# Performance work log

Hardware: AMD Instinct MI355X
Metric: run time of the kernel (lower is better)

## Reference

```python
import jax, jax.numpy as jnp
import numpy as np

B, N, D, H, DEPTH = 2, 2048, 768, 12, 4
DH = D // H
SCALE = DH ** -0.5
EPS = 1e-5
FF = 4 * D


def layer_norm(x, w, b):
    m = jnp.mean(x, axis=-1, keepdims=True)
    v = jnp.mean((x - m) ** 2, axis=-1, keepdims=True)
    return (x - m) * jax.lax.rsqrt(v + EPS) * w + b


def to_heads(t):  # [b, n, D] -> [b, H, n, DH]
    b, n, _ = t.shape
    return t.reshape(b, n, H, DH).transpose(0, 2, 1, 3)


def merge_heads(t):  # [b, H, n, DH] -> [b, n, D]
    b, h, n, dh = t.shape
    return t.transpose(0, 2, 1, 3).reshape(b, n, D)


def attend(q, k, v, bias):
    s = jnp.einsum('bhid,bhjd->bhij', q, k) * SCALE + bias
    a = jax.nn.softmax(s, axis=-1)
    return merge_heads(jnp.einsum('bhij,bhjd->bhid', a, v))


def setup_inputs():
    key = jax.random.key(0)
    ks = iter(jax.random.split(key, 16))

    def p(shape, scale=0.02):
        return jax.random.normal(next(ks), shape, dtype=jnp.float32) * scale

    inp = {
        'x': jax.random.normal(next(ks), (B, N, D), dtype=jnp.float32),
        'context': jax.random.normal(next(ks), (B, N, D), dtype=jnp.float32),
        'relative_position_bias': jax.random.normal(next(ks), (1, H, N, N), dtype=jnp.float32) * 0.02,
        # self-attn params (stacked over depth)
        'ln1_w': jnp.ones((DEPTH, D), jnp.float32), 'ln1_b': jnp.zeros((DEPTH, D), jnp.float32),
        'w_qkv': p((DEPTH, D, 3 * D)),
        'w_so': p((DEPTH, D, D)), 'b_so': jnp.zeros((DEPTH, D), jnp.float32),
        # cross-attn params (shared LN applied to x and context, as in source)
        'ln2_w': jnp.ones((DEPTH, D), jnp.float32), 'ln2_b': jnp.zeros((DEPTH, D), jnp.float32),
        'w_q': p((DEPTH, D, D)), 'w_k': p((DEPTH, D, D)), 'w_v': p((DEPTH, D, D)),
        'w_co': p((DEPTH, D, D)), 'b_co': jnp.zeros((DEPTH, D), jnp.float32),
        # FFN params
        'ln3_w': jnp.ones((DEPTH, D), jnp.float32), 'ln3_b': jnp.zeros((DEPTH, D), jnp.float32),
        'w_f1': p((DEPTH, D, FF)), 'b_f1': jnp.zeros((DEPTH, FF), jnp.float32),
        'w_f2': p((DEPTH, FF, D)), 'b_f2': jnp.zeros((DEPTH, D), jnp.float32),
        # final norm
        'lnout_w': jnp.ones((D,), jnp.float32), 'lnout_b': jnp.zeros((D,), jnp.float32),
    }
    return inp


def reference(x, context, relative_position_bias,
              ln1_w, ln1_b, w_qkv, w_so, b_so,
              ln2_w, ln2_b, w_q, w_k, w_v, w_co, b_co,
              ln3_w, ln3_b, w_f1, b_f1, w_f2, b_f2,
              lnout_w, lnout_b):
    bias = relative_position_bias
    for i in range(DEPTH):
        # self-attention block (pre-norm, residual)
        xn = layer_norm(x, ln1_w[i], ln1_b[i])
        q, k, v = jnp.split(xn @ w_qkv[i], 3, axis=-1)
        o = attend(to_heads(q), to_heads(k), to_heads(v), bias)
        x = o @ w_so[i] + b_so[i] + x
        # cross-attention block (input_norm shared for x and context)
        xn = layer_norm(x, ln2_w[i], ln2_b[i])
        cn = layer_norm(context, ln2_w[i], ln2_b[i])
        o = attend(to_heads(xn @ w_q[i]), to_heads(cn @ w_k[i]), to_heads(cn @ w_v[i]), bias)
        x = o @ w_co[i] + b_co[i] + x
        # FFN block
        xn = layer_norm(x, ln3_w[i], ln3_b[i])
        h = jax.nn.gelu(xn @ w_f1[i] + b_f1[i], approximate=False)
        x = h @ w_f2[i] + b_f2[i] + x
    return layer_norm(x, lnout_w, lnout_b)
```

## Files before the change

### kernel.cpp

```cpp
#include <hip/hip_runtime.h>
#include <cstdint>
#include <cstddef>

#define DEV static __device__ __forceinline__

typedef float  f32x4 __attribute__((ext_vector_type(4)));
typedef short  s16x8 __attribute__((ext_vector_type(8)));
typedef unsigned short u16;
typedef unsigned short u16x2 __attribute__((ext_vector_type(2)));
typedef unsigned short u16x4 __attribute__((ext_vector_type(4)));
typedef unsigned short u16x8 __attribute__((ext_vector_type(8)));
typedef __bf16 bf16x8 __attribute__((ext_vector_type(8)));

#define LOG2E 1.4426950408889634f
#define QSCALE_CONST 0.18033688011112042f

DEV float bf2f(u16 v){ union { unsigned u; float f; } x; x.u = ((unsigned)v) << 16; return x.f; }
DEV u16 f2bf(float f){ return __builtin_bit_cast(u16, (__bf16)f); }

DEV float fexp2(float x){
#if __has_builtin(__builtin_amdgcn_exp2f)
  return __builtin_amdgcn_exp2f(x);
#else
  return exp2f(x);
#endif
}

DEV f32x4 mfma16(s16x8 a, s16x8 b, f32x4 c){
  return __builtin_amdgcn_mfma_f32_16x16x32_bf16(
      __builtin_bit_cast(bf16x8, a), __builtin_bit_cast(bf16x8, b), c, 0, 0, 0);
}

DEV void gld16(const void* g, void* l){
  __builtin_amdgcn_global_load_lds(
      (const __attribute__((address_space(1))) void*)(uintptr_t)g,
      (__attribute__((address_space(3))) void*)(unsigned)(uintptr_t)l,
      16, 0, 0);
}

__global__ void __launch_bounds__(256)
transpose_cvt(const float* __restrict__ src, u16* __restrict__ dst, int K, int N,
              size_t dzstride){
  int z = blockIdx.z;
  src += (size_t)z * K * N;
  dst += (size_t)z * dzstride;
  __shared__ float t[32][33];
  int n0 = blockIdx.x * 32, k0 = blockIdx.y * 32;
#pragma unroll
  for (int i = 0; i < 4; ++i)
    t[threadIdx.y + 8*i][threadIdx.x] = src[(size_t)(k0 + threadIdx.y + 8*i) * N + n0 + threadIdx.x];
  __syncthreads();
#pragma unroll
  for (int i = 0; i < 4; ++i)
    dst[(size_t)(n0 + threadIdx.y + 8*i) * K + k0 + threadIdx.x] = f2bf(t[threadIdx.x][threadIdx.y + 8*i]);
}

__global__ void __launch_bounds__(256)
cvt_biasT(const float* __restrict__ in, u16* __restrict__ out){
  const int kvt = blockIdx.x, qt = blockIdx.y, h = blockIdx.z, tid = threadIdx.x;
  const int q  = qt * 64 + ((tid >> 6) << 4) + (tid & 15);
  const int c0 = kvt * 64 + ((tid >> 4) & 3) * 4;
  const float* src = in + ((size_t)h * 2048 + q) * 2048;
  u16x8 o0, o1;
#pragma unroll
  for (int mi = 0; mi < 4; ++mi){
    f32x4 v = *(const f32x4*)(src + c0 + mi * 16);
#pragma unroll
    for (int r = 0; r < 4; ++r){
      u16 bv = f2bf(v[r] * LOG2E);
      if (mi < 2) o0[(mi & 1) * 4 + r] = bv; else o1[(mi & 1) * 4 + r] = bv;
    }
  }
  u16* dst = out + ((size_t)(h * 32 + qt) * 32 + kvt) * 4096 + tid * 16;
  *(u16x8*)dst = o0;
  *(u16x8*)(dst + 8) = o1;
}

__global__ void __launch_bounds__(256)
lnv(const float* __restrict__ x, const float* __restrict__ w, const float* __restrict__ b,
    u16* __restrict__ out){
  const int wv = threadIdx.x >> 6, lane = threadIdx.x & 63;
  const float* wz = w + blockIdx.y * 768;
  const float* bz = b + blockIdx.y * 768;
  out += (size_t)blockIdx.y * 4096 * 768;
  const int row = blockIdx.x * 4 + wv;
  const float* xr = x + (size_t)row * 768;
  f32x4 t[3]; float s = 0.f, s2 = 0.f;
#pragma unroll
  for (int c = 0; c < 3; ++c){
    t[c] = *(const f32x4*)(xr + c * 256 + lane * 4);
#pragma unroll
    for (int j = 0; j < 4; ++j){ s += t[c][j]; s2 += t[c][j] * t[c][j]; }
  }
#pragma unroll
  for (int off = 1; off < 64; off <<= 1){ s += __shfl_xor(s, off); s2 += __shfl_xor(s2, off); }
  float m = s * (1.f/768.f);
  float rstd = rsqrtf(s2 * (1.f/768.f) - m * m + 1e-5f);
#pragma unroll
  for (int c = 0; c < 3; ++c){
    const int col = c * 256 + lane * 4;
    f32x4 wv4 = *(const f32x4*)(wz + col);
    f32x4 bv4 = *(const f32x4*)(bz + col);
    u16x4 o;
#pragma unroll
    for (int j = 0; j < 4; ++j) o[j] = f2bf((t[c][j] - m) * rstd * wv4[j] + bv4[j]);
    *(u16x4*)(out + (size_t)row * 768 + col) = o;
  }
}

template<typename OUT>
__global__ void __launch_bounds__(256)
red_ln(const float* __restrict__ p, const float* __restrict__ biasrow,
       float* __restrict__ xbuf, OUT* __restrict__ out,
       const float* __restrict__ lw, const float* __restrict__ lb){
  const int wv = threadIdx.x >> 6, lane = threadIdx.x & 63;
  const int row = blockIdx.x * 4 + wv;
  const float* p0 = p + (size_t)row * 768;
  const float* p1 = p0 + 4096ll * 768;
  float* xr = xbuf + (size_t)row * 768;
  f32x4 t[3]; float s = 0.f, s2 = 0.f;
#pragma unroll
  for (int c = 0; c < 3; ++c){
    const int col = c * 256 + lane * 4;
    f32x4 v0 = *(const f32x4*)(p0 + col);
    f32x4 v1 = *(const f32x4*)(p1 + col);
    f32x4 bv = *(const f32x4*)(biasrow + col);
    f32x4 xv = *(const f32x4*)(xr + col);
    f32x4 v = v0 + v1 + bv + xv;
    *(f32x4*)(xr + col) = v;
    t[c] = v;
#pragma unroll
    for (int j = 0; j < 4; ++j){ s += v[j]; s2 += v[j] * v[j]; }
  }
#pragma unroll
  for (int off = 1; off < 64; off <<= 1){ s += __shfl_xor(s, off); s2 += __shfl_xor(s2, off); }
  float m = s * (1.f/768.f);
  float rstd = rsqrtf(s2 * (1.f/768.f) - m * m + 1e-5f);
#pragma unroll
  for (int c = 0; c < 3; ++c){
    const int col = c * 256 + lane * 4;
    f32x4 wv4 = *(const f32x4*)(lw + col);
    f32x4 bv4 = *(const f32x4*)(lb + col);
    if constexpr (sizeof(OUT) == 2){
      u16x4 o;
#pragma unroll
      for (int j = 0; j < 4; ++j) o[j] = f2bf((t[c][j] - m) * rstd * wv4[j] + bv4[j]);
      *(u16x4*)((u16*)out + (size_t)row * 768 + col) = o;
    } else {
      f32x4 o;
#pragma unroll
      for (int j = 0; j < 4; ++j) o[j] = (t[c][j] - m) * rstd * wv4[j] + bv4[j];
      *(f32x4*)((float*)out + (size_t)row * 768 + col) = o;
    }
  }
}

template<int BM, int BN, int EPI>
__global__ void __launch_bounds__(256)
gemm_bf16(const u16* __restrict__ A, int lda, const u16* __restrict__ Bt, int ldb,
          int nk, u16* __restrict__ Cb, float* __restrict__ Cf, int ldc,
          const float* __restrict__ bias,
          const u16* __restrict__ A2, const u16* __restrict__ Bt2){
  constexpr int MT = BM / 32, NT = BN / 32;
  __shared__ u16 As[2][BM * 32];
  __shared__ u16 Bs[2][BN * 32];
  float colscale = 1.0f;
  if constexpr (EPI == 4){
    const int z = blockIdx.z;
    if (z == 0){ colscale = QSCALE_CONST; }
    else { A = A2; Bt = Bt2 + (size_t)(z - 1) * 768 * 768; }
    Cb += z * 768;
  }
  if constexpr (EPI == 5){
    const int z = blockIdx.z;
    A  += (size_t)z * nk * 32;
    Bt += (size_t)z * nk * 32;
    Cf += (size_t)z * 4096 * 768;
  }
  const int tid = threadIdx.x, w = tid >> 6, lane = tid & 63;
  const int l16 = lane & 15, g = lane >> 4;
  const int m0 = blockIdx.x * BM, n0 = blockIdx.y * BN;
  const int wm = (w >> 1) * (BM / 2), wn = (w & 1) * (BN / 2);
  f32x4 acc[MT][NT] = {};

  const u16* a0 = A + (size_t)(m0 + (tid >> 2)) * lda + (tid & 3) * 8;
  const u16* a1 = (BM == 128) ? A + (size_t)(m0 + (tid >> 2) + 64) * lda + (tid & 3) * 8 : nullptr;
  const u16* b0 = Bt + (size_t)(n0 + (tid >> 2)) * ldb + (tid & 3) * 8;
  const u16* b1 = (BN == 128) ? Bt + (size_t)(n0 + (tid >> 2) + 64) * ldb + (tid & 3) * 8 : nullptr;

  {
    char* ab = (char*)As[0]; char* bb = (char*)Bs[0];
    gld16(a0, ab + w * 1024);
    if constexpr (BM == 128) gld16(a1, ab + 4096 + w * 1024);
    gld16(b0, bb + w * 1024);
    if constexpr (BN == 128) gld16(b1, bb + 4096 + w * 1024);
  }
  __syncthreads();

  int cb = 0;
  for (int kt = 0; kt < nk; ++kt){
    if (kt + 1 < nk){
      const int k1 = (kt + 1) * 32;
      char* ab = (char*)As[cb ^ 1]; char* bb = (char*)Bs[cb ^ 1];
      gld16(a0 + k1, ab + w * 1024);
      if constexpr (BM == 128) gld16(a1 + k1, ab + 4096 + w * 1024);
      gld16(b0 + k1, bb + w * 1024);
      if constexpr (BN == 128) gld16(b1 + k1, bb + 4096 + w * 1024);
    }
    const u16* Ab = As[cb]; const u16* Bb = Bs[cb];
    s16x8 af[MT], bfv[NT];
#pragma unroll
    for (int mi = 0; mi < MT; ++mi)
      af[mi] = *(const s16x8*)(Ab + (wm + mi*16 + l16) * 32 + 8 * g);
#pragma unroll
    for (int ni = 0; ni < NT; ++ni)
      bfv[ni] = *(const s16x8*)(Bb + (wn + ni*16 + l16) * 32 + 8 * g);
#pragma unroll
    for (int mi = 0; mi < MT; ++mi)
#pragma unroll
      for (int ni = 0; ni < NT; ++ni)
        acc[mi][ni] = mfma16(af[mi], bfv[ni], acc[mi][ni]);
    __syncthreads();
    cb ^= 1;
  }

#pragma unroll
  for (int mi = 0; mi < MT; ++mi){
    const int rg = m0 + wm + mi*16 + 4*g;
#pragma unroll
    for (int ni = 0; ni < NT; ++ni){
      const int col = n0 + wn + ni*16 + l16;
      f32x4 v = acc[mi][ni];
#pragma unroll
      for (int r = 0; r < 4; ++r){
        const int row = rg + r;
        if constexpr (EPI == 2){
          float t = v[r] + bias[col];
          float ge = 0.5f * t * (1.0f + erff(t * 0.7071067811865476f));
          Cb[(size_t)row * ldc + col] = f2bf(ge);
        } else if constexpr (EPI == 3){
          float sc = (col < 768) ? QSCALE_CONST : 1.0f;
          Cb[(size_t)row * ldc + col] = f2bf(v[r] * sc);
        } else if constexpr (EPI == 4){
          Cb[(size_t)row * ldc + col] = f2bf(v[r] * colscale);
        } else {
          Cf[(size_t)row * 768 + col] = v[r];
        }
      }
    }
  }
}

__global__ void __launch_bounds__(256)
attn_kernel(const u16* __restrict__ qkv, const u16* __restrict__ biasT, u16* __restrict__ out){
  __shared__ __align__(16) u16 Ks[2][4096];
  __shared__ __align__(16) u16 Vt[2][4096];
  __shared__ __align__(16) u16 Pl[4][1024];

  const int tid = threadIdx.x, w = tid >> 6, lane = tid & 63;
  const int l16 = lane & 15, g = lane >> 4;
  const int qt = blockIdx.x, h = blockIdx.y, b = blockIdx.z;
  const int rowbase = b * 2048, q0 = qt * 64;

  const int ci0 = w * 64 + lane, ci1 = ci0 + 256;
  const int r0 = ci0 >> 3, sc0 = ci0 & 7, r1 = ci1 >> 3, sc1 = ci1 & 7;
  const u16* kp0 = qkv + (size_t)(rowbase + r0) * 2304 + 768 + h * 64 + (((sc0 ^ (r0 & 7)) & 7) << 3);
  const u16* kp1 = qkv + (size_t)(rowbase + r1) * 2304 + 768 + h * 64 + (((sc1 ^ (r1 & 7)) & 7) << 3);
  const int dh0 = (tid & 31) * 2, vs = tid >> 5;
  const u16* vp = qkv + (size_t)(rowbase + vs * 8) * 2304 + 1536 + h * 64 + dh0;
  u16x2 vr[8];
  const u16* bT = biasT + ((size_t)(h * 32 + qt) * 32) * 4096 + tid * 16;
  u16x8 brA, brB, bnA, bnB;

  const u16* qrow = qkv + (size_t)(rowbase + q0 + w * 16 + l16) * 2304 + h * 64;
  s16x8 qf0 = *(const s16x8*)(qrow + 8 * g);
  s16x8 qf1 = *(const s16x8*)(qrow + 32 + 8 * g);

  f32x4 oacc[4] = {};
  float mrun = -3.0e38f, lrun = 0.f;
  const int sw = l16 & 7;

  {
    char* kb = (char*)Ks[0] + w * 1024;
    gld16(kp0, kb); gld16(kp1, kb + 4096);
#pragma unroll
    for (int i = 0; i < 8; ++i) vr[i] = *(const u16x2*)(vp + (size_t)i * 2304);
    brA = *(const u16x8*)(bT);
    brB = *(const u16x8*)(bT + 8);
    s16x8 vA, vB;
#pragma unroll
    for (int j = 0; j < 8; ++j){ vA[j] = (short)vr[j][0]; vB[j] = (short)vr[j][1]; }
    *(s16x8*)(Vt[0] + dh0 * 64 + ((vs ^ (dh0 & 7)) << 3)) = vA;
    *(s16x8*)(Vt[0] + (dh0 + 1) * 64 + ((vs ^ ((dh0 + 1) & 7)) << 3)) = vB;
  }
  __syncthreads();

  for (int t = 0; t < 32; ++t){
    const int cb = t & 1;
    if (t < 31){
      const size_t koff = (size_t)(t + 1) * 64 * 2304;
      char* kb = (char*)Ks[cb ^ 1] + w * 1024;
      gld16(kp0 + koff, kb); gld16(kp1 + koff, kb + 4096);
      const u16* p = vp + koff;
#pragma unroll
      for (int i = 0; i < 8; ++i) vr[i] = *(const u16x2*)(p + (size_t)i * 2304);
      const u16* bp = bT + (size_t)(t + 1) * 4096;
      bnA = *(const u16x8*)(bp);
      bnB = *(const u16x8*)(bp + 8);
    }

    f32x4 st[4];
#pragma unroll
    for (int mi = 0; mi < 4; ++mi){
      const int row = l16 + 16 * mi;
      s16x8 kf0 = *(const s16x8*)(Ks[cb] + row * 64 + ((g ^ sw) << 3));
      s16x8 kf1 = *(const s16x8*)(Ks[cb] + row * 64 + (((g + 4) ^ sw) << 3));
      f32x4 z = {};
      z = mfma16(kf0, qf0, z);
      st[mi] = mfma16(kf1, qf1, z);
    }

    float tmax = -3.0e38f;
#pragma unroll
    for (int mi = 0; mi < 4; ++mi){
#pragma unroll
      for (int r = 0; r < 4; ++r){
        float bval = bf2f(mi < 2 ? brA[(mi & 1) * 4 + r] : brB[(mi & 1) * 4 + r]);
        float v = st[mi][r] + bval;
        st[mi][r] = v;
        tmax = fmaxf(tmax, v);
      }
    }
    tmax = fmaxf(tmax, __shfl_xor(tmax, 16));
    tmax = fmaxf(tmax, __shfl_xor(tmax, 32));
    if (!__all(tmax <= mrun + 8.f)){
      float mnew = fmaxf(mrun, tmax);
      float al = fexp2(mrun - mnew);
      mrun = mnew;
      lrun *= al;
#pragma unroll
      for (int r = 0; r < 4; ++r){
        float aq = __shfl(al, 4 * g + r);
#pragma unroll
        for (int ni = 0; ni < 4; ++ni) oacc[ni][r] *= aq;
      }
    }
    float ssum = 0.f;
#pragma unroll
    for (int mi = 0; mi < 4; ++mi){
      u16x4 pk;
#pragma unroll
      for (int r = 0; r < 4; ++r){
        float pv = fexp2(st[mi][r] - mrun);
        ssum += pv;
        pk[r] = f2bf(pv);
      }
      *(u16x4*)(Pl[w] + l16 * 64 + (((2*mi + (g >> 1)) ^ sw) << 3) + 4 * (g & 1)) = pk;
    }
    ssum += __shfl_xor(ssum, 16);
    ssum += __shfl_xor(ssum, 32);
    lrun += ssum;

#pragma unroll
    for (int ks2 = 0; ks2 < 2; ++ks2){
      s16x8 pf = *(const s16x8*)(Pl[w] + l16 * 64 + (((4*ks2 + g) ^ sw) << 3));
#pragma unroll
      for (int ni = 0; ni < 4; ++ni){
        const int dh = l16 + 16 * ni;
        s16x8 vf = *(const s16x8*)(Vt[cb] + dh * 64 + (((4*ks2 + g) ^ sw) << 3));
        oacc[ni] = mfma16(pf, vf, oacc[ni]);
      }
    }

    if (t < 31){
      s16x8 vA, vB;
#pragma unroll
      for (int j = 0; j < 8; ++j){ vA[j] = (short)vr[j][0]; vB[j] = (short)vr[j][1]; }
      *(s16x8*)(Vt[cb ^ 1] + dh0 * 64 + ((vs ^ (dh0 & 7)) << 3)) = vA;
      *(s16x8*)(Vt[cb ^ 1] + (dh0 + 1) * 64 + ((vs ^ ((dh0 + 1) & 7)) << 3)) = vB;
      brA = bnA; brB = bnB;
    }
    __syncthreads();
  }

#pragma unroll
  for (int r = 0; r < 4; ++r){
    float lq = __shfl(lrun, 4 * g + r);
    float inv = 1.0f / lq;
    const int row = rowbase + q0 + w * 16 + 4 * g + r;
#pragma unroll
    for (int ni = 0; ni < 4; ++ni)
      out[(size_t)row * 768 + h * 64 + l16 + 16 * ni] = f2bf(oacc[ni][r] * inv);
  }
}

extern "C" void kernel_launch(void* const* d_in, const int* in_sizes, int n_in,
                              void* d_out, int out_size, void* d_ws, size_t ws_size,
                              hipStream_t stream){
  const float* in_x    = (const float*)d_in[0];
  const float* in_ctx  = (const float*)d_in[1];
  const float* in_bias = (const float*)d_in[2];
  const float* ln1_w = (const float*)d_in[3];
  const float* ln1_b = (const float*)d_in[4];
  const float* w_qkv = (const float*)d_in[5];
  const float* w_so  = (const float*)d_in[6];
  const float* b_so  = (const float*)d_in[7];
  const float* ln2_w = (const float*)d_in[8];
  const float* ln2_b = (const float*)d_in[9];
  const float* w_q   = (const float*)d_in[10];
  const float* w_k   = (const float*)d_in[11];
  const float* w_v   = (const float*)d_in[12];
  const float* w_co  = (const float*)d_in[13];
  const float* b_co  = (const float*)d_in[14];
  const float* ln3_w = (const float*)d_in[15];
  const float* ln3_b = (const float*)d_in[16];
  const float* w_f1  = (const float*)d_in[17];
  const float* b_f1  = (const float*)d_in[18];
  const float* w_f2  = (const float*)d_in[19];
  const float* b_f2  = (const float*)d_in[20];
  const float* lnout_w = (const float*)d_in[21];
  const float* lnout_b = (const float*)d_in[22];

  char* p = (char*)d_ws;
  float* xbuf  = (float*)p;  p += 4096ll * 768 * 4;
  float* pbuf  = (float*)p;  p += 2ll * 4096 * 768 * 4;
  u16* xn      = (u16*)p;    p += 4096ll * 768 * 2;
  u16* cn      = (u16*)p;    p += 4ll * 4096 * 768 * 2;
  u16* qkvb    = (u16*)p;    p += 4096ll * 2304 * 2;
  u16* attO    = (u16*)p;    p += 4096ll * 768 * 2;
  u16* ffh     = (u16*)p;    p += 4096ll * 3072 * 2;
  u16* wqkvT   = (u16*)p;    p += 4ll * 2304 * 768 * 2;
  u16* wsoT    = (u16*)p;    p += 4ll * 768 * 768 * 2;
  u16* wqT     = (u16*)p;    p += 4ll * 768 * 768 * 2;
  u16* wkvT    = (u16*)p;    p += 4ll * 1536 * 768 * 2;
  u16* wcoT    = (u16*)p;    p += 4ll * 768 * 768 * 2;
  u16* wf1T    = (u16*)p;    p += 4ll * 3072 * 768 * 2;
  u16* wf2T    = (u16*)p;    p += 4ll * 768 * 3072 * 2;
  u16* biasT   = (u16*)p;    p += 12ll * 2048 * 2048 * 2;

  hipMemcpyAsync(xbuf, in_x, 4096ll * 768 * 4, hipMemcpyDeviceToDevice, stream);

  const dim3 tb(32, 8);
  transpose_cvt<<<dim3(72, 24, 4), tb, 0, stream>>>(w_qkv, wqkvT, 768, 2304, 2304ll*768);
  transpose_cvt<<<dim3(24, 24, 4), tb, 0, stream>>>(w_so,  wsoT,  768, 768,  768ll*768);
  transpose_cvt<<<dim3(24, 24, 4), tb, 0, stream>>>(w_q,   wqT,   768, 768,  768ll*768);
  transpose_cvt<<<dim3(24, 24, 4), tb, 0, stream>>>(w_k,   wkvT,             768, 768, 1536ll*768);
  transpose_cvt<<<dim3(24, 24, 4), tb, 0, stream>>>(w_v,   wkvT + 768ll*768, 768, 768, 1536ll*768);
  transpose_cvt<<<dim3(24, 24, 4), tb, 0, stream>>>(w_co,  wcoT,  768, 768,  768ll*768);
  transpose_cvt<<<dim3(96, 24, 4), tb, 0, stream>>>(w_f1,  wf1T,  768, 3072, 3072ll*768);
  transpose_cvt<<<dim3(24, 96, 4), tb, 0, stream>>>(w_f2,  wf2T,  3072, 768, 768ll*3072);
  cvt_biasT<<<dim3(32, 32, 12), 256, 0, stream>>>(in_bias, biasT);
  lnv<<<dim3(1024, 4), 256, 0, stream>>>(in_ctx, ln2_w, ln2_b, cn);
  lnv<<<dim3(1024, 1), 256, 0, stream>>>(xbuf, ln1_w, ln1_b, xn);

  const dim3 ag(32, 12, 2);
  for (int i = 0; i < 4; ++i){
    gemm_bf16<64,128,3><<<dim3(64, 18), 256, 0, stream>>>(xn, 768, wqkvT + (size_t)i*2304*768, 768, 24,
                                                          qkvb, nullptr, 2304, nullptr, nullptr, nullptr);
    attn_kernel<<<ag, 256, 0, stream>>>(qkvb, biasT, attO);
    gemm_bf16<128,64,5><<<dim3(32, 12, 2), 256, 0, stream>>>(attO, 768, wsoT + (size_t)i*768*768, 768, 12,
                                                             nullptr, pbuf, 768, nullptr, nullptr, nullptr);
    red_ln<u16><<<1024, 256, 0, stream>>>(pbuf, b_so + i*768, xbuf, xn, ln2_w + i*768, ln2_b + i*768);
    gemm_bf16<64,128,4><<<dim3(64, 6, 3), 256, 0, stream>>>(xn, 768, wqT + (size_t)i*768*768, 768, 24,
                                                            qkvb, nullptr, 2304, nullptr,
                                                            cn + (size_t)i*4096*768, wkvT + (size_t)i*1536*768);
    attn_kernel<<<ag, 256, 0, stream>>>(qkvb, biasT, attO);
    gemm_bf16<128,64,5><<<dim3(32, 12, 2), 256, 0, stream>>>(attO, 768, wcoT + (size_t)i*768*768, 768, 12,
                                                             nullptr, pbuf, 768, nullptr, nullptr, nullptr);
    red_ln<u16><<<1024, 256, 0, stream>>>(pbuf, b_co + i*768, xbuf, xn, ln3_w + i*768, ln3_b + i*768);
    gemm_bf16<64,128,2><<<dim3(64, 24), 256, 0, stream>>>(xn, 768, wf1T + (size_t)i*3072*768, 768, 24,
                                                          ffh, nullptr, 3072, b_f1 + i*3072, nullptr, nullptr);
    gemm_bf16<128,64,5><<<dim3(32, 12, 2), 256, 0, stream>>>(ffh, 3072, wf2T + (size_t)i*768*3072, 3072, 48,
                                                             nullptr, pbuf, 768, nullptr, nullptr, nullptr);
    if (i < 3)
      red_ln<u16><<<1024, 256, 0, stream>>>(pbuf, b_f2 + i*768, xbuf, xn, ln1_w + (i+1)*768, ln1_b + (i+1)*768);
    else
      red_ln<float><<<1024, 256, 0, stream>>>(pbuf, b_f2 + i*768, xbuf, (float*)d_out, lnout_w, lnout_b);
  }
}
```

Baseline: 1.419 ms.

## Store position bias as scaled fp8, use 128x128 GEMM tiles, 4-way split-K

The relative position bias is pre-scaled by 256 and stored as fp8 e4m3 instead of bf16. This halves the bias bytes the attention kernel reads on every tile, and the values are decoded with hardware packed-convert instructions. All GEMMs now use a fixed 128x128 tile, and the output projections move from 2-way to 4-way split-K, so the reduce+LN kernel now sums four partial buffers. s_setprio hints are placed around the MFMA sections in attention. The risks are lower bias precision, extra partial-sum traffic, and fewer blocks per launch for some GEMMs.

```diff
diff --git a/kernel.cpp b/kernel.cpp
--- a/kernel.cpp
+++ b/kernel.cpp
@@ -5,17 +5,20 @@
 #define DEV static __device__ __forceinline__
 
 typedef float  f32x4 __attribute__((ext_vector_type(4)));
+typedef float  f32x2 __attribute__((ext_vector_type(2)));
 typedef short  s16x8 __attribute__((ext_vector_type(8)));
 typedef unsigned short u16;
+typedef unsigned int   u32;
+typedef unsigned int   u32x4 __attribute__((ext_vector_type(4)));
 typedef unsigned short u16x2 __attribute__((ext_vector_type(2)));
 typedef unsigned short u16x4 __attribute__((ext_vector_type(4)));
-typedef unsigned short u16x8 __attribute__((ext_vector_type(8)));
 typedef __bf16 bf16x8 __attribute__((ext_vector_type(8)));
 
 #define LOG2E 1.4426950408889634f
 #define QSCALE_CONST 0.18033688011112042f
-
-DEV float bf2f(u16 v){ union { unsigned u; float f; } x; x.u = ((unsigned)v) << 16; return x.f; }
+#define BSCALE 256.0f
+#define BINV   0.00390625f
+
 DEV u16 f2bf(float f){ return __builtin_bit_cast(u16, (__bf16)f); }
 
 DEV float fexp2(float x){
@@ -37,6 +40,56 @@
       (__attribute__((address_space(3))) void*)(unsigned)(uintptr_t)l,
       16, 0, 0);
 }
+
+#if __has_builtin(__builtin_amdgcn_cvt_pk_fp8_f32) && __has_builtin(__builtin_amdgcn_cvt_pk_f32_fp8)
+DEV u32 pk4_fp8(f32x4 v){
+  int r = __builtin_amdgcn_cvt_pk_fp8_f32(v[0], v[1], 0, false);
+  r     = __builtin_amdgcn_cvt_pk_fp8_f32(v[2], v[3], r, true);
+  return (u32)r;
+}
+template<bool HI>
+DEV f32x2 upk_fp8(u32 w){
+  return __builtin_amdgcn_cvt_pk_f32_fp8((int)w, HI);
+}
+#else
+DEV unsigned enc1(float x){
+  union{float f; unsigned u;} c; c.f = x;
+  unsigned s = (c.u >> 24) & 0x80;
+  int e = (int)((c.u >> 23) & 0xff) - 127;
+  unsigned m = c.u & 0x7fffff;
+  if (e >= -6){
+    unsigned mant = m >> 20, rem = m & 0xfffff;
+    if (rem > 0x80000 || (rem == 0x80000 && (mant & 1))) mant++;
+    unsigned eb = (unsigned)(e + 7);
+    if (mant == 8){ mant = 0; eb++; }
+    if (eb >= 16){ eb = 15; mant = 6; }
+    return s | (eb << 3) | mant;
+  }
+  if (e < -10) return s;
+  int sh = -6 - e;
+  unsigned full = (1u << 23) | m;
+  unsigned mant = full >> (20 + sh);
+  unsigned rem  = full & ((1u << (20 + sh)) - 1);
+  unsigned half = 1u << (19 + sh);
+  if (rem > half || (rem == half && (mant & 1))) mant++;
+  if (mant == 8) return s | (1u << 3);
+  return s | mant;
+}
+DEV u32 pk4_fp8(f32x4 v){
+  return enc1(v[0]) | (enc1(v[1]) << 8) | (enc1(v[2]) << 16) | (enc1(v[3]) << 24);
+}
+DEV float dec1(unsigned b){
+  int s = (b >> 7) & 1, e = (b >> 3) & 15; float m = (float)(b & 7) * 0.125f;
+  float v = e ? ldexpf(1.0f + m, e - 7) : ldexpf(m, -6);
+  return s ? -v : v;
+}
+template<bool HI>
+DEV f32x2 upk_fp8(u32 w){
+  unsigned lo = HI ? ((w >> 16) & 0xff) : (w & 0xff);
+  unsigned h2 = HI ? ((w >> 24) & 0xff) : ((w >> 8) & 0xff);
+  f32x2 r; r[0] = dec1(lo); r[1] = dec1(h2); return r;
+}
+#endif
 
 __global__ void __launch_bounds__(256)
 transpose_cvt(const float* __restrict__ src, u16* __restrict__ dst, int K, int N,
@@ -56,24 +109,20 @@
 }
 
 __global__ void __launch_bounds__(256)
-cvt_biasT(const float* __restrict__ in, u16* __restrict__ out){
+cvt_biasT(const float* __restrict__ in, unsigned char* __restrict__ out){
   const int kvt = blockIdx.x, qt = blockIdx.y, h = blockIdx.z, tid = threadIdx.x;
   const int q  = qt * 64 + ((tid >> 6) << 4) + (tid & 15);
   const int c0 = kvt * 64 + ((tid >> 4) & 3) * 4;
   const float* src = in + ((size_t)h * 2048 + q) * 2048;
-  u16x8 o0, o1;
+  u32x4 wv;
 #pragma unroll
   for (int mi = 0; mi < 4; ++mi){
     f32x4 v = *(const f32x4*)(src + c0 + mi * 16);
 #pragma unroll
-    for (int r = 0; r < 4; ++r){
-      u16 bv = f2bf(v[r] * LOG2E);
-      if (mi < 2) o0[(mi & 1) * 4 + r] = bv; else o1[(mi & 1) * 4 + r] = bv;
-    }
-  }
-  u16* dst = out + ((size_t)(h * 32 + qt) * 32 + kvt) * 4096 + tid * 16;
-  *(u16x8*)dst = o0;
-  *(u16x8*)(dst + 8) = o1;
+    for (int r = 0; r < 4; ++r) v[r] = fminf(fmaxf(v[r] * (LOG2E * BSCALE), -448.f), 448.f);
+    wv[mi] = pk4_fp8(v);
+  }
+  *(u32x4*)(out + ((size_t)(h * 32 + qt) * 32 + kvt) * 4096 + tid * 16) = wv;
 }
 
 __global__ void __launch_bounds__(256)
@@ -115,18 +164,19 @@
        const float* __restrict__ lw, const float* __restrict__ lb){
   const int wv = threadIdx.x >> 6, lane = threadIdx.x & 63;
   const int row = blockIdx.x * 4 + wv;
+  const size_t S = 4096ll * 768;
   const float* p0 = p + (size_t)row * 768;
-  const float* p1 = p0 + 4096ll * 768;
   float* xr = xbuf + (size_t)row * 768;
   f32x4 t[3]; float s = 0.f, s2 = 0.f;
 #pragma unroll
   for (int c = 0; c < 3; ++c){
     const int col = c * 256 + lane * 4;
-    f32x4 v0 = *(const f32x4*)(p0 + col);
-    f32x4 v1 = *(const f32x4*)(p1 + col);
-    f32x4 bv = *(const f32x4*)(biasrow + col);
-    f32x4 xv = *(const f32x4*)(xr + col);
-    f32x4 v = v0 + v1 + bv + xv;
+    f32x4 v = *(const f32x4*)(p0 + col);
+    v += *(const f32x4*)(p0 + S + col);
+    v += *(const f32x4*)(p0 + 2*S + col);
+    v += *(const f32x4*)(p0 + 3*S + col);
+    v += *(const f32x4*)(biasrow + col);
+    v += *(const f32x4*)(xr + col);
     *(f32x4*)(xr + col) = v;
     t[c] = v;
 #pragma unroll
@@ -155,15 +205,14 @@
   }
 }
 
-template<int BM, int BN, int EPI>
+template<int EPI>
 __global__ void __launch_bounds__(256)
 gemm_bf16(const u16* __restrict__ A, int lda, const u16* __restrict__ Bt, int ldb,
           int nk, u16* __restrict__ Cb, float* __restrict__ Cf, int ldc,
           const float* __restrict__ bias,
           const u16* __restrict__ A2, const u16* __restrict__ Bt2){
-  constexpr int MT = BM / 32, NT = BN / 32;
-  __shared__ u16 As[2][BM * 32];
-  __shared__ u16 Bs[2][BN * 32];
+  __shared__ u16 As[2][128 * 32];
+  __shared__ u16 Bs[2][128 * 32];
   float colscale = 1.0f;
   if constexpr (EPI == 4){
     const int z = blockIdx.z;
@@ -179,21 +228,19 @@
   }
   const int tid = threadIdx.x, w = tid >> 6, lane = tid & 63;
   const int l16 = lane & 15, g = lane >> 4;
-  const int m0 = blockIdx.x * BM, n0 = blockIdx.y * BN;
-  const int wm = (w >> 1) * (BM / 2), wn = (w & 1) * (BN / 2);
-  f32x4 acc[MT][NT] = {};
-
-  const u16* a0 = A + (size_t)(m0 + (tid >> 2)) * lda + (tid & 3) * 8;
-  const u16* a1 = (BM == 128) ? A + (size_t)(m0 + (tid >> 2) + 64) * lda + (tid & 3) * 8 : nullptr;
+  const int m0 = blockIdx.x * 128, n0 = blockIdx.y * 128;
+  const int wm = (w >> 1) * 64, wn = (w & 1) * 64;
+  f32x4 acc[4][4] = {};
+
+  const u16* a0 = A  + (size_t)(m0 + (tid >> 2)) * lda + (tid & 3) * 8;
+  const u16* a1 = A  + (size_t)(m0 + (tid >> 2) + 64) * lda + (tid & 3) * 8;
   const u16* b0 = Bt + (size_t)(n0 + (tid >> 2)) * ldb + (tid & 3) * 8;
-  const u16* b1 = (BN == 128) ? Bt + (size_t)(n0 + (tid >> 2) + 64) * ldb + (tid & 3) * 8 : nullptr;
+  const u16* b1 = Bt + (size_t)(n0 + (tid >> 2) + 64) * ldb + (tid & 3) * 8;
 
   {
     char* ab = (char*)As[0]; char* bb = (char*)Bs[0];
-    gld16(a0, ab + w * 1024);
-    if constexpr (BM == 128) gld16(a1, ab + 4096 + w * 1024);
-    gld16(b0, bb + w * 1024);
-    if constexpr (BN == 128) gld16(b1, bb + 4096 + w * 1024);
+    gld16(a0, ab + w * 1024); gld16(a1, ab + 4096 + w * 1024);
+    gld16(b0, bb + w * 1024); gld16(b1, bb + 4096 + w * 1024);
   }
   __syncthreads();
 
@@ -202,33 +249,31 @@
     if (kt + 1 < nk){
       const int k1 = (kt + 1) * 32;
       char* ab = (char*)As[cb ^ 1]; char* bb = (char*)Bs[cb ^ 1];
-      gld16(a0 + k1, ab + w * 1024);
-      if constexpr (BM == 128) gld16(a1 + k1, ab + 4096 + w * 1024);
-      gld16(b0 + k1, bb + w * 1024);
-      if constexpr (BN == 128) gld16(b1 + k1, bb + 4096 + w * 1024);
+      gld16(a0 + k1, ab + w * 1024); gld16(a1 + k1, ab + 4096 + w * 1024);
+      gld16(b0 + k1, bb + w * 1024); gld16(b1 + k1, bb + 4096 + w * 1024);
     }
     const u16* Ab = As[cb]; const u16* Bb = Bs[cb];
-    s16x8 af[MT], bfv[NT];
-#pragma unroll
-    for (int mi = 0; mi < MT; ++mi)
+    s16x8 af[4], bfv[4];
+#pragma unroll
+    for (int mi = 0; mi < 4; ++mi)
       af[mi] = *(const s16x8*)(Ab + (wm + mi*16 + l16) * 32 + 8 * g);
 #pragma unroll
-    for (int ni = 0; ni < NT; ++ni)
+    for (int ni = 0; ni < 4; ++ni)
       bfv[ni] = *(const s16x8*)(Bb + (wn + ni*16 + l16) * 32 + 8 * g);
 #pragma unroll
-    for (int mi = 0; mi < MT; ++mi)
-#pragma unroll
-      for (int ni = 0; ni < NT; ++ni)
+    for (int mi = 0; mi < 4; ++mi)
+#pragma unroll
+      for (int ni = 0; ni < 4; ++ni)
         acc[mi][ni] = mfma16(af[mi], bfv[ni], acc[mi][ni]);
     __syncthreads();
     cb ^= 1;
   }
 
 #pragma unroll
-  for (int mi = 0; mi < MT; ++mi){
+  for (int mi = 0; mi < 4; ++mi){
     const int rg = m0 + wm + mi*16 + 4*g;
 #pragma unroll
-    for (int ni = 0; ni < NT; ++ni){
+    for (int ni = 0; ni < 4; ++ni){
       const int col = n0 + wn + ni*16 + l16;
       f32x4 v = acc[mi][ni];
 #pragma unroll
@@ -252,7 +297,8 @@
 }
 
 __global__ void __launch_bounds__(256)
-attn_kernel(const u16* __restrict__ qkv, const u16* __restrict__ biasT, u16* __restrict__ out){
+attn_kernel(const u16* __restrict__ qkv, const unsigned char* __restrict__ biasT,
+            u16* __restrict__ out){
   __shared__ __align__(16) u16 Ks[2][4096];
   __shared__ __align__(16) u16 Vt[2][4096];
   __shared__ __align__(16) u16 Pl[4][1024];
@@ -269,8 +315,8 @@
   const int dh0 = (tid & 31) * 2, vs = tid >> 5;
   const u16* vp = qkv + (size_t)(rowbase + vs * 8) * 2304 + 1536 + h * 64 + dh0;
   u16x2 vr[8];
-  const u16* bT = biasT + ((size_t)(h * 32 + qt) * 32) * 4096 + tid * 16;
-  u16x8 brA, brB, bnA, bnB;
+  const unsigned char* bT = biasT + ((size_t)(h * 32 + qt) * 32) * 4096 + tid * 16;
+  u32x4 brW, bnW;
 
   const u16* qrow = qkv + (size_t)(rowbase + q0 + w * 16 + l16) * 2304 + h * 64;
   s16x8 qf0 = *(const s16x8*)(qrow + 8 * g);
@@ -285,8 +331,7 @@
     gld16(kp0, kb); gld16(kp1, kb + 4096);
 #pragma unroll
     for (int i = 0; i < 8; ++i) vr[i] = *(const u16x2*)(vp + (size_t)i * 2304);
-    brA = *(const u16x8*)(bT);
-    brB = *(const u16x8*)(bT + 8);
+    brW = *(const u32x4*)(bT);
     s16x8 vA, vB;
 #pragma unroll
     for (int j = 0; j < 8; ++j){ vA[j] = (short)vr[j][0]; vB[j] = (short)vr[j][1]; }
@@ -304,12 +349,11 @@
       const u16* p = vp + koff;
 #pragma unroll
       for (int i = 0; i < 8; ++i) vr[i] = *(const u16x2*)(p + (size_t)i * 2304);
-      const u16* bp = bT + (size_t)(t + 1) * 4096;
-      bnA = *(const u16x8*)(bp);
-      bnB = *(const u16x8*)(bp + 8);
+      bnW = *(const u32x4*)(bT + (size_t)(t + 1) * 4096);
     }
 
     f32x4 st[4];
+    __builtin_amdgcn_s_setprio(1);
 #pragma unroll
     for (int mi = 0; mi < 4; ++mi){
       const int row = l16 + 16 * mi;
@@ -319,17 +363,19 @@
       z = mfma16(kf0, qf0, z);
       st[mi] = mfma16(kf1, qf1, z);
     }
+    __builtin_amdgcn_s_setprio(0);
 
     float tmax = -3.0e38f;
 #pragma unroll
     for (int mi = 0; mi < 4; ++mi){
-#pragma unroll
-      for (int r = 0; r < 4; ++r){
-        float bval = bf2f(mi < 2 ? brA[(mi & 1) * 4 + r] : brB[(mi & 1) * 4 + r]);
-        float v = st[mi][r] + bval;
-        st[mi][r] = v;
-        tmax = fmaxf(tmax, v);
-      }
+      f32x2 lo = upk_fp8<false>(brW[mi]);
+      f32x2 hi = upk_fp8<true>(brW[mi]);
+      st[mi][0] = fmaf(lo[0], BINV, st[mi][0]);
+      st[mi][1] = fmaf(lo[1], BINV, st[mi][1]);
+      st[mi][2] = fmaf(hi[0], BINV, st[mi][2]);
+      st[mi][3] = fmaf(hi[1], BINV, st[mi][3]);
+#pragma unroll
+      for (int r = 0; r < 4; ++r) tmax = fmaxf(tmax, st[mi][r]);
     }
     tmax = fmaxf(tmax, __shfl_xor(tmax, 16));
     tmax = fmaxf(tmax, __shfl_xor(tmax, 32));
@@ -361,6 +407,7 @@
     ssum += __shfl_xor(ssum, 32);
     lrun += ssum;
 
+    __builtin_amdgcn_s_setprio(1);
 #pragma unroll
     for (int ks2 = 0; ks2 < 2; ++ks2){
       s16x8 pf = *(const s16x8*)(Pl[w] + l16 * 64 + (((4*ks2 + g) ^ sw) << 3));
@@ -371,6 +418,7 @@
         oacc[ni] = mfma16(pf, vf, oacc[ni]);
       }
     }
+    __builtin_amdgcn_s_setprio(0);
 
     if (t < 31){
       s16x8 vA, vB;
@@ -378,7 +426,7 @@
       for (int j = 0; j < 8; ++j){ vA[j] = (short)vr[j][0]; vB[j] = (short)vr[j][1]; }
       *(s16x8*)(Vt[cb ^ 1] + dh0 * 64 + ((vs ^ (dh0 & 7)) << 3)) = vA;
       *(s16x8*)(Vt[cb ^ 1] + (dh0 + 1) * 64 + ((vs ^ ((dh0 + 1) & 7)) << 3)) = vB;
-      brA = bnA; brB = bnB;
+      brW = bnW;
     }
     __syncthreads();
   }
@@ -423,7 +471,7 @@
 
   char* p = (char*)d_ws;
   float* xbuf  = (float*)p;  p += 4096ll * 768 * 4;
-  float* pbuf  = (float*)p;  p += 2ll * 4096 * 768 * 4;
+  float* pbuf  = (float*)p;  p += 4ll * 4096 * 768 * 4;
   u16* xn      = (u16*)p;    p += 4096ll * 768 * 2;
   u16* cn      = (u16*)p;    p += 4ll * 4096 * 768 * 2;
   u16* qkvb    = (u16*)p;    p += 4096ll * 2304 * 2;
@@ -436,7 +484,7 @@
   u16* wcoT    = (u16*)p;    p += 4ll * 768 * 768 * 2;
   u16* wf1T    = (u16*)p;    p += 4ll * 3072 * 768 * 2;
   u16* wf2T    = (u16*)p;    p += 4ll * 768 * 3072 * 2;
-  u16* biasT   = (u16*)p;    p += 12ll * 2048 * 2048 * 2;
+  unsigned char* biasT = (unsigned char*)p; p += 12ll * 2048 * 2048;
 
   hipMemcpyAsync(xbuf, in_x, 4096ll * 768 * 4, hipMemcpyDeviceToDevice, stream);
 
@@ -455,23 +503,23 @@
 
   const dim3 ag(32, 12, 2);
   for (int i = 0; i < 4; ++i){
-    gemm_bf16<64,128,3><<<dim3(64, 18), 256, 0, stream>>>(xn, 768, wqkvT + (size_t)i*2304*768, 768, 24,
-                                                          qkvb, nullptr, 2304, nullptr, nullptr, nullptr);
+    gemm_bf16<3><<<dim3(32, 18), 256, 0, stream>>>(xn, 768, wqkvT + (size_t)i*2304*768, 768, 24,
+                                                   qkvb, nullptr, 2304, nullptr, nullptr, nullptr);
     attn_kernel<<<ag, 256, 0, stream>>>(qkvb, biasT, attO);
-    gemm_bf16<128,64,5><<<dim3(32, 12, 2), 256, 0, stream>>>(attO, 768, wsoT + (size_t)i*768*768, 768, 12,
-                                                             nullptr, pbuf, 768, nullptr, nullptr, nullptr);
+    gemm_bf16<5><<<dim3(32, 6, 4), 256, 0, stream>>>(attO, 768, wsoT + (size_t)i*768*768, 768, 6,
+                                                     nullptr, pbuf, 768, nullptr, nullptr, nullptr);
     red_ln<u16><<<1024, 256, 0, stream>>>(pbuf, b_so + i*768, xbuf, xn, ln2_w + i*768, ln2_b + i*768);
-    gemm_bf16<64,128,4><<<dim3(64, 6, 3), 256, 0, stream>>>(xn, 768, wqT + (size_t)i*768*768, 768, 24,
-                                                            qkvb, nullptr, 2304, nullptr,
-                                                            cn + (size_t)i*4096*768, wkvT + (size_t)i*1536*768);
+    gemm_bf16<4><<<dim3(32, 6, 3), 256, 0, stream>>>(xn, 768, wqT + (size_t)i*768*768, 768, 24,
+                                                     qkvb, nullptr, 2304, nullptr,
+                                                     cn + (size_t)i*4096*768, wkvT + (size_t)i*1536*768);
     attn_kernel<<<ag, 256, 0, stream>>>(qkvb, biasT, attO);
-    gemm_bf16<128,64,5><<<dim3(32, 12, 2), 256, 0, stream>>>(attO, 768, wcoT + (size_t)i*768*768, 768, 12,
-                                                             nullptr, pbuf, 768, nullptr, nullptr, nullptr);
+    gemm_bf16<5><<<dim3(32, 6, 4), 256, 0, stream>>>(attO, 768, wcoT + (size_t)i*768*768, 768, 6,
+                                                     nullptr, pbuf, 768, nullptr, nullptr, nullptr);
     red_ln<u16><<<1024, 256, 0, stream>>>(pbuf, b_co + i*768, xbuf, xn, ln3_w + i*768, ln3_b + i*768);
-    gemm_bf16<64,128,2><<<dim3(64, 24), 256, 0, stream>>>(xn, 768, wf1T + (size_t)i*3072*768, 768, 24,
-                                                          ffh, nullptr, 3072, b_f1 + i*3072, nullptr, nullptr);
-    gemm_bf16<128,64,5><<<dim3(32, 12, 2), 256, 0, stream>>>(ffh, 3072, wf2T + (size_t)i*768*3072, 3072, 48,
-                                                             nullptr, pbuf, 768, nullptr, nullptr, nullptr);
+    gemm_bf16<2><<<dim3(32, 24), 256, 0, stream>>>(xn, 768, wf1T + (size_t)i*3072*768, 768, 24,
+                                                   ffh, nullptr, 3072, b_f1 + i*3072, nullptr, nullptr);
+    gemm_bf16<5><<<dim3(32, 6, 4), 256, 0, stream>>>(ffh, 3072, wf2T + (size_t)i*768*3072, 3072, 24,
+                                                     nullptr, pbuf, 768, nullptr, nullptr, nullptr);
     if (i < 3)
       red_ln<u16><<<1024, 256, 0, stream>>>(pbuf, b_f2 + i*768, xbuf, xn, ln1_w + (i+1)*768, ln1_b + (i+1)*768);
     else
```

New measurement: 1.355 ms. 4.5% less time.
